# Optimization experiments

Measured on AMD Instinct MI355X. Metric: run time of the kernel, lower is better.

## Reference

```python
import jax, jax.numpy as jnp
import numpy as np

N = 50000        # nodes
E_RAND = 800000  # random edges (self-loops appended -> E = 850000)
H = 8            # num_heads
D = 32           # h_feat_dim
IN = 128         # in_feat_dim
SM = 256         # sm_dim
SP = 128         # sp_dim
NEG_SLOPE = 0.2  # DGL GATv2Conv default


def setup_inputs() -> dict:
    key = jax.random.key(0)
    ks = jax.random.split(key, 16)
    s = 0.05
    self_loops = jnp.arange(N, dtype=jnp.int32)
    return {
        "sm_feats": jax.random.normal(ks[0], (N, SM), jnp.float32),
        "sp_feats": jax.random.normal(ks[1], (N, SP), jnp.float32),
        "src": jnp.concatenate([jax.random.randint(ks[2], (E_RAND,), 0, N, jnp.int32), self_loops]),
        "dst": jnp.concatenate([jax.random.randint(ks[3], (E_RAND,), 0, N, jnp.int32), self_loops]),
        # T1 / T2 linears
        "T1_w": jax.random.normal(ks[4], (SM, IN), jnp.float32) * s,
        "T1_b": jnp.zeros((IN,), jnp.float32),
        "T2_w": jax.random.normal(ks[5], (SP, IN), jnp.float32) * s,
        "T2_b": jnp.zeros((IN,), jnp.float32),
        # GATv2 layer 1: in = 2*IN
        "g1_src_w": jax.random.normal(ks[6], (2 * IN, H * D), jnp.float32) * s,
        "g1_dst_w": jax.random.normal(ks[7], (2 * IN, H * D), jnp.float32) * s,
        "g1_attn": jax.random.normal(ks[8], (H, D), jnp.float32) * s,
        "g1_bias": jnp.zeros((H * D,), jnp.float32),
        # GATv2 layer 2: in = D (after head-mean)
        "g2_src_w": jax.random.normal(ks[9], (D, H * D), jnp.float32) * s,
        "g2_dst_w": jax.random.normal(ks[10], (D, H * D), jnp.float32) * s,
        "g2_attn": jax.random.normal(ks[11], (H, D), jnp.float32) * s,
        "g2_bias": jnp.zeros((H * D,), jnp.float32),
    }


def gatv2_conv(x, src, dst, w_src, w_dst, attn, bias):
    # DGL GATv2Conv (share_weights=False, bias=True, no residual/activation)
    feat_src = (x @ w_src).reshape(-1, H, D)   # [N,H,D]
    feat_dst = (x @ w_dst).reshape(-1, H, D)   # [N,H,D]
    e = jax.nn.leaky_relu(feat_src[src] + feat_dst[dst], NEG_SLOPE)  # [E,H,D]
    score = jnp.einsum('ehd,hd->eh', e, attn)  # [E,H]
    # edge softmax over incoming edges per destination (self-loops ensure non-empty)
    smax = jax.ops.segment_max(score, dst, num_segments=N)           # [N,H]
    ex = jnp.exp(score - smax[dst])
    denom = jax.ops.segment_sum(ex, dst, num_segments=N)             # [N,H]
    alpha = ex / denom[dst]                                          # [E,H]
    out = jax.ops.segment_sum(alpha[:, :, None] * feat_src[src], dst, num_segments=N)  # [N,H,D]
    return out + bias.reshape(1, H, D)


def reference(sm_feats, sp_feats, src, dst,
              T1_w, T1_b, T2_w, T2_b,
              g1_src_w, g1_dst_w, g1_attn, g1_bias,
              g2_src_w, g2_dst_w, g2_attn, g2_bias):
    in_feat = jnp.concatenate([sm_feats @ T1_w + T1_b,
                               sp_feats @ T2_w + T2_b], axis=1)      # [N, 2*IN]
    h = gatv2_conv(in_feat, src, dst, g1_src_w, g1_dst_w, g1_attn, g1_bias)
    h = jax.nn.elu(h).mean(axis=1)                                   # [N, D]
    h = gatv2_conv(h, src, dst, g2_src_w, g2_dst_w, g2_attn, g2_bias)
    return h.mean(axis=1)                                            # [N, D]
```

## Files before the change

kernel.cpp:

```cpp
#include <hip/hip_runtime.h>
#include <hip/hip_fp16.h>


typedef unsigned int uint32;
typedef unsigned short u16;
typedef float f32x4 __attribute__((ext_vector_type(4)));
typedef _Float16 f16x2 __attribute__((ext_vector_type(2)));
typedef _Float16 f16x8 __attribute__((ext_vector_type(8)));

union H2 { f16x2 v; uint32 u; };

__device__ __forceinline__ int wave_incl_scan(int x) {
  int lane = threadIdx.x & 63;
#pragma unroll
  for (int off = 1; off < 64; off <<= 1) {
    int t = __shfl_up(x, off, 64);
    if (lane >= off) x += t;
  }
  return x;
}

__global__ __launch_bounds__(256) void k_deg(const int* __restrict__ dst, int* __restrict__ deg, int E) {
  int e = blockIdx.x * 256 + threadIdx.x;
  if (e < E) atomicAdd(&deg[dst[e]], 1);
}

__global__ __launch_bounds__(256) void k_blkscan(const int* __restrict__ in, int* __restrict__ out,
                                                 int* __restrict__ blksum, int n) {
  __shared__ int wsum[4];
  int tid = threadIdx.x;
  int i0 = blockIdx.x * 1024 + tid * 4;
  int v0 = 0, v1 = 0, v2 = 0, v3 = 0;
  if (i0 + 3 < n) {
    int4 t = *(const int4*)(in + i0);
    v0 = t.x; v1 = t.y; v2 = t.z; v3 = t.w;
  } else {
    if (i0 < n) v0 = in[i0];
    if (i0 + 1 < n) v1 = in[i0 + 1];
    if (i0 + 2 < n) v2 = in[i0 + 2];
    if (i0 + 3 < n) v3 = in[i0 + 3];
  }
  int ts = v0 + v1 + v2 + v3;
  int incl = wave_incl_scan(ts);
  int lane = tid & 63, wid = tid >> 6;
  if (lane == 63) wsum[wid] = incl;
  __syncthreads();
  if (tid == 0) {
    int a = wsum[0], b = wsum[1], c = wsum[2], d = wsum[3];
    wsum[0] = 0; wsum[1] = a; wsum[2] = a + b; wsum[3] = a + b + c;
    blksum[blockIdx.x] = a + b + c + d;
  }
  __syncthreads();
  int excl = wsum[wid] + incl - ts;
  if (i0 + 3 < n) {
    int4 o; o.x = excl; o.y = excl + v0; o.z = excl + v0 + v1; o.w = excl + v0 + v1 + v2;
    *(int4*)(out + i0) = o;
  } else {
    if (i0 < n) out[i0] = excl;
    if (i0 + 1 < n) out[i0 + 1] = excl + v0;
    if (i0 + 2 < n) out[i0 + 2] = excl + v0 + v1;
    if (i0 + 3 < n) out[i0 + 3] = excl + v0 + v1 + v2;
  }
}

__global__ void k_scan_top(int* __restrict__ bs, int G) {
  int lane = threadIdx.x;
  int base = 0;
  for (int s = 0; s < G; s += 64) {
    int i = s + lane;
    int v = (i < G) ? bs[i] : 0;
    int incl = wave_incl_scan(v);
    if (i < G) bs[i] = base + incl - v;
    base += __shfl(incl, 63, 64);
  }
}

__global__ __launch_bounds__(256) void k_addoff(int* __restrict__ rp, const int* __restrict__ bs, int n, int Etot) {
  int i = blockIdx.x * 256 + threadIdx.x;
  if (i < n) rp[i] += bs[i >> 10];
  if (i == 0) rp[n] = Etot;
}

__global__ __launch_bounds__(256) void k_fill(const int* __restrict__ src, const int* __restrict__ dst,
                                              const int* __restrict__ rp, int* __restrict__ cnt,
                                              int* __restrict__ csr_src, int E) {
  int e = blockIdx.x * 256 + threadIdx.x;
  if (e < E) {
    int d = dst[e];
    int p = rp[d] + atomicAdd(&cnt[d], 1);
    csr_src[p] = src[e];
  }
}

__global__ __launch_bounds__(256) void k_precomb(const float* __restrict__ T1w, const float* __restrict__ T1b,
                                                 const float* __restrict__ T2w, const float* __restrict__ T2b,
                                                 const float* __restrict__ G1, const float* __restrict__ G2,
                                                 __half* __restrict__ Bf, float* __restrict__ cvec) {
  int bb = blockIdx.x;
  const float* G = (bb < 385) ? G1 : G2;
  int off = (bb < 385) ? 0 : 256;
  int r = (bb < 385) ? bb : bb - 385;
  int j = threadIdx.x;
  float acc = 0.f;
  if (r < 256) {
    for (int m = 0; m < 128; m++) acc += T1w[r * 128 + m] * G[m * 256 + j];
  } else if (r < 384) {
    int rr = r - 256;
    for (int m = 0; m < 128; m++) acc += T2w[rr * 128 + m] * G[(128 + m) * 256 + j];
  } else {
    for (int m = 0; m < 128; m++) acc += T1b[m] * G[m * 256 + j] + T2b[m] * G[(128 + m) * 256 + j];
    cvec[off + j] = acc;
    return;
  }
  int k = r, colabs = off + j;
  int kt = k >> 5, lq = (k >> 3) & 3, j8 = k & 7;
  int cb = colabs >> 7, colr = colabs & 127, ni = colr >> 4, lr = colr & 15;
  size_t idx = ((size_t)(((cb * 12 + kt) * 8 + ni) * 4 + lq) * 16 + lr) * 8 + j8;
  Bf[idx] = __float2half(acc);
}

#define GLL(GP, LP)                                                     \
  __builtin_amdgcn_global_load_lds(                                     \
      (const __attribute__((address_space(1))) void*)(GP),              \
      (__attribute__((address_space(3))) void*)(LP), 16, 0, 0)

__global__ __launch_bounds__(256, 4) void k_gemm(const float* __restrict__ sm, const float* __restrict__ sp,
                                                 const u16* __restrict__ Bf, const float* __restrict__ cvec,
                                                 __half* __restrict__ fs, __half* __restrict__ fd, int N) {
  __shared__ u16 BFl[3 * 4096];
  int tid = threadIdx.x, w = tid >> 6, l = tid & 63;
  int lr = l & 15, lq = l >> 4;
  int L = blockIdx.x;
  int x = L & 7, m = L >> 3;
  int cb = m & 3;
  int rb = x + 8 * (m >> 2);
  int col0 = cb * 128, row0 = rb * 128;
  if (row0 >= N) return;
  int r0 = row0 + w * 32 + lr;
  int r1 = r0 + 16;
  int c0 = r0 < N ? r0 : N - 1;
  int c1 = r1 < N ? r1 : N - 1;
  const float* psm0 = sm + (size_t)c0 * 256 + lq * 8;
  const float* psm1 = sm + (size_t)c1 * 256 + lq * 8;
  const float* psp0 = sp + (size_t)c0 * 128 + lq * 8;
  const float* psp1 = sp + (size_t)c1 * 128 + lq * 8;

  f32x4 acc[2][8];
#pragma unroll
  for (int mt = 0; mt < 2; mt++)
#pragma unroll
    for (int ni = 0; ni < 8; ni++) acc[mt][ni] = (f32x4){0.f, 0.f, 0.f, 0.f};

#define STAGE_B(S, BUF)                                                 \
  {                                                                     \
    size_t g0 = (size_t)(cb * 12 + (S)) * 4096;                         \
    _Pragma("unroll") for (int i = 0; i < 2; i++) {                     \
      int c = i * 256 + tid;                                            \
      int lb = (BUF)*4096 + (i * 4 + w) * 512;                          \
      GLL(Bf + g0 + (size_t)c * 8, &BFl[lb]);                           \
    }                                                                   \
  }

#define LOADA(P, D)                                                     \
  {                                                                     \
    const float* _g0 = ((P) < 8) ? (psm0 + (P)*32) : (psp0 + ((P)-8) * 32); \
    const float* _g1 = ((P) < 8) ? (psm1 + (P)*32) : (psp1 + ((P)-8) * 32); \
    D[0] = *(const float4*)_g0;                                         \
    D[1] = *(const float4*)(_g0 + 4);                                   \
    D[2] = *(const float4*)_g1;                                         \
    D[3] = *(const float4*)(_g1 + 4);                                   \
  }

  float4 Aa[4], Ab[4];
  LOADA(0, Aa);
  STAGE_B(0, 0);
  STAGE_B(1, 1);
  asm volatile("s_waitcnt vmcnt(2)" ::: "memory");
  __builtin_amdgcn_sched_barrier(0);
  __builtin_amdgcn_s_barrier();

#pragma unroll
  for (int st = 0; st < 12; st++) {
    const int slot = st % 3;
    const float4* Dc = (st & 1) ? Ab : Aa;
    float4* Dn = (st & 1) ? Aa : Ab;
    if (st < 11) LOADA(st + 1, Dn);
    if (st < 10) STAGE_B(st + 2, (st + 2) % 3);
    f16x8 a0, a1;
    a0[0] = (_Float16)Dc[0].x; a0[1] = (_Float16)Dc[0].y;
    a0[2] = (_Float16)Dc[0].z; a0[3] = (_Float16)Dc[0].w;
    a0[4] = (_Float16)Dc[1].x; a0[5] = (_Float16)Dc[1].y;
    a0[6] = (_Float16)Dc[1].z; a0[7] = (_Float16)Dc[1].w;
    a1[0] = (_Float16)Dc[2].x; a1[1] = (_Float16)Dc[2].y;
    a1[2] = (_Float16)Dc[2].z; a1[3] = (_Float16)Dc[2].w;
    a1[4] = (_Float16)Dc[3].x; a1[5] = (_Float16)Dc[3].y;
    a1[6] = (_Float16)Dc[3].z; a1[7] = (_Float16)Dc[3].w;
#pragma unroll
    for (int ni = 0; ni < 8; ni++) {
      int lo = slot * 4096 + (ni * 64 + l) * 8;
      f16x8 bf = *(const f16x8*)&BFl[lo];
      acc[0][ni] = __builtin_amdgcn_mfma_f32_16x16x32_f16(a0, bf, acc[0][ni], 0, 0, 0);
      acc[1][ni] = __builtin_amdgcn_mfma_f32_16x16x32_f16(a1, bf, acc[1][ni], 0, 0, 0);
    }
    if (st < 10) {
      asm volatile("s_waitcnt vmcnt(6)" ::: "memory");
    } else if (st == 10) {
      asm volatile("s_waitcnt vmcnt(4)" ::: "memory");
    }
    if (st < 11) {
      __builtin_amdgcn_sched_barrier(0);
      __builtin_amdgcn_s_barrier();
    }
  }

#pragma unroll
  for (int mt = 0; mt < 2; mt++) {
    int rbr = row0 + w * 32 + mt * 16 + lq * 4;
#pragma unroll
    for (int ni = 0; ni < 8; ni++) {
      int c = col0 + ni * 16 + lr;
      float cv = cvec[c];
      __half* op = fs; int cc = c;
      if (c >= 256) { op = fd; cc = c - 256; }
#pragma unroll
      for (int r = 0; r < 4; r++) {
        int rr = rbr + r;
        if (rr < N) op[(size_t)rr * 256 + cc] = __float2half(acc[mt][ni][r] + cv);
      }
    }
  }
#undef STAGE_B
#undef LOADA
}

__global__ __launch_bounds__(256) void k_feat2(const float* __restrict__ h, const float* __restrict__ Ws,
                                               const float* __restrict__ Wd, __half* __restrict__ fs,
                                               __half* __restrict__ fd, int N) {
  int j = threadIdx.x;
  int n0 = blockIdx.x * 32;
  float ws[32], wd[32];
#pragma unroll
  for (int k = 0; k < 32; k++) {
    ws[k] = Ws[k * 256 + j];
    wd[k] = Wd[k * 256 + j];
  }
  int nend = n0 + 32; if (nend > N) nend = N;
#pragma unroll 2
  for (int n = n0; n < nend; n++) {
    const float* hr = h + (size_t)n * 32;
    float as = 0.f, ad = 0.f;
#pragma unroll
    for (int k = 0; k < 32; k++) {
      float hv = hr[k];
      as += hv * ws[k];
      ad += hv * wd[k];
    }
    fs[(size_t)n * 256 + j] = __float2half(as);
    fd[(size_t)n * 256 + j] = __float2half(ad);
  }
}

template <int FINAL>
__global__ __launch_bounds__(256) void k_edge(const uint4* __restrict__ fs4, const uint4* __restrict__ fd4,
                                              const int* __restrict__ csr_src, const int* __restrict__ rp,
                                              const float* __restrict__ attn, const float* __restrict__ bias,
                                              float* __restrict__ out, int N) {
  int n = blockIdx.x * 4 + (threadIdx.x >> 6);
  if (n >= N) return;
  int lane = threadIdx.x & 63;
  int lh = lane & 31;
  float4 a0 = ((const float4*)attn)[lh * 2];
  float4 a1 = ((const float4*)attn)[lh * 2 + 1];
  H2 AV01, AV23, AV45, AV67;
  AV01.v = (f16x2){(_Float16)a0.x, (_Float16)a0.y};
  AV23.v = (f16x2){(_Float16)a0.z, (_Float16)a0.w};
  AV45.v = (f16x2){(_Float16)a1.x, (_Float16)a1.y};
  AV67.v = (f16x2){(_Float16)a1.z, (_Float16)a1.w};
  const f16x2 c02 = {(_Float16)0.2f, (_Float16)0.2f};
  uint4 yu = fd4[(size_t)n * 32 + lh];
  H2 Y01, Y23, Y45, Y67;
  Y01.u = yu.x; Y23.u = yu.y; Y45.u = yu.z; Y67.u = yu.w;
  int beg = rp[n], end = rp[n + 1];
  float den = 0.f;
  float acc[8] = {0.f, 0.f, 0.f, 0.f, 0.f, 0.f, 0.f, 0.f};

  auto pair1 = [&](uint4 xu, bool tail) {
    H2 Xa, Xb, Xc, Xd;
    Xa.u = xu.x; Xb.u = xu.y; Xc.u = xu.z; Xd.u = xu.w;
    f16x2 e0 = Xa.v + Y01.v, e1 = Xb.v + Y23.v, e2 = Xc.v + Y45.v, e3 = Xd.v + Y67.v;
    f16x2 t0 = __builtin_elementwise_max(e0, e0 * c02);
    f16x2 t1 = __builtin_elementwise_max(e1, e1 * c02);
    f16x2 t2 = __builtin_elementwise_max(e2, e2 * c02);
    f16x2 t3 = __builtin_elementwise_max(e3, e3 * c02);
    float p = __builtin_amdgcn_fdot2(t0, AV01.v, 0.f, false);
    p = __builtin_amdgcn_fdot2(t1, AV23.v, p, false);
    p = __builtin_amdgcn_fdot2(t2, AV45.v, p, false);
    p = __builtin_amdgcn_fdot2(t3, AV67.v, p, false);
    p += __shfl_xor(p, 1, 64);
    p += __shfl_xor(p, 2, 64);
    float wgt = __expf(p);
    if (tail && lane >= 32) wgt = 0.f;
    den += wgt;
    acc[0] += wgt * (float)Xa.v.x; acc[1] += wgt * (float)Xa.v.y;
    acc[2] += wgt * (float)Xb.v.x; acc[3] += wgt * (float)Xb.v.y;
    acc[4] += wgt * (float)Xc.v.x; acc[5] += wgt * (float)Xc.v.y;
    acc[6] += wgt * (float)Xd.v.x; acc[7] += wgt * (float)Xd.v.y;
  };

  int e = beg;
  int np = (end - beg) >> 1;
  if (np > 0) {
    int sA = csr_src[e], sB = csr_src[e + 1];
    int s = (lane < 32) ? sA : sB;
    uint4 xcur = fs4[(size_t)s * 32 + lh];
    for (int q = 1; q < np; q++) {
      int eb = e + 2 * q;
      int tA = csr_src[eb], tB = csr_src[eb + 1];
      int t = (lane < 32) ? tA : tB;
      uint4 xnext = fs4[(size_t)t * 32 + lh];
      pair1(xcur, false);
      xcur = xnext;
    }
    pair1(xcur, false);
    e += 2 * np;
  }
  if (e < end) {
    int sA = csr_src[e];
    uint4 xu = fs4[(size_t)sA * 32 + lh];
    pair1(xu, true);
  }

  den += __shfl_xor(den, 32, 64);
#pragma unroll
  for (int j = 0; j < 8; j++) acc[j] += __shfl_xor(acc[j], 32, 64);
  float invd = 1.f / den;
  float4 b0 = ((const float4*)bias)[lh * 2];
  float4 b1 = ((const float4*)bias)[lh * 2 + 1];
  float bj[8] = {b0.x, b0.y, b0.z, b0.w, b1.x, b1.y, b1.z, b1.w};
#pragma unroll
  for (int j = 0; j < 8; j++) {
    float v = acc[j] * invd + bj[j];
    if (!FINAL) v = v > 0.f ? v : expm1f(v);
    acc[j] = v;
  }
#pragma unroll
  for (int mask = 4; mask <= 16; mask <<= 1)
#pragma unroll
    for (int j = 0; j < 8; j++) acc[j] += __shfl_xor(acc[j], mask, 64);
  if (lane < 4) {
    float4 o0 = {acc[0] * 0.125f, acc[1] * 0.125f, acc[2] * 0.125f, acc[3] * 0.125f};
    float4 o1 = {acc[4] * 0.125f, acc[5] * 0.125f, acc[6] * 0.125f, acc[7] * 0.125f};
    ((float4*)out)[(size_t)n * 8 + lane * 2] = o0;
    ((float4*)out)[(size_t)n * 8 + lane * 2 + 1] = o1;
  }
}

extern "C" void kernel_launch(void* const* d_in, const int* in_sizes, int n_in,
                              void* d_out, int out_size, void* d_ws, size_t ws_size,
                              hipStream_t stream) {
  const float* sm  = (const float*)d_in[0];
  const float* sp  = (const float*)d_in[1];
  const int*   src = (const int*)d_in[2];
  const int*   dst = (const int*)d_in[3];
  const float* T1w = (const float*)d_in[4];
  const float* T1b = (const float*)d_in[5];
  const float* T2w = (const float*)d_in[6];
  const float* T2b = (const float*)d_in[7];
  const float* g1sw = (const float*)d_in[8];
  const float* g1dw = (const float*)d_in[9];
  const float* g1a  = (const float*)d_in[10];
  const float* g1b  = (const float*)d_in[11];
  const float* g2sw = (const float*)d_in[12];
  const float* g2dw = (const float*)d_in[13];
  const float* g2a  = (const float*)d_in[14];
  const float* g2b  = (const float*)d_in[15];
  const int N = in_sizes[1] / 128;
  const int E = in_sizes[2];
  float* out = (float*)d_out;

  size_t off = 0;
  char* wsb = (char*)d_ws;
  auto alloc = [&](size_t bytes) -> void* {
    void* p = wsb + off;
    off += (bytes + 255) & ~(size_t)255;
    return p;
  };
  __half* Bf  = (__half*)alloc((size_t)512 * 384 * 2);
  float* cvec  = (float*)alloc(512 * 4);
  int* deg     = (int*)alloc((size_t)N * 4);
  int* cnt     = (int*)alloc((size_t)N * 4);
  int* row_ptr = (int*)alloc((size_t)(N + 1) * 4);
  int* blksum  = (int*)alloc(4096 * 4);
  int* csr_src = (int*)alloc((size_t)E * 4);
  __half* fs   = (__half*)alloc((size_t)N * 256 * 2);
  __half* fd   = (__half*)alloc((size_t)N * 256 * 2);
  float* hmid  = (float*)alloc((size_t)N * 32 * 4);
  (void)ws_size; (void)n_in; (void)out_size;

  (void)hipMemsetAsync(deg, 0, (size_t)N * 4, stream);
  (void)hipMemsetAsync(cnt, 0, (size_t)N * 4, stream);

  k_deg<<<(E + 255) / 256, 256, 0, stream>>>(dst, deg, E);
  int nblk = (N + 1023) / 1024;
  k_blkscan<<<nblk, 256, 0, stream>>>(deg, row_ptr, blksum, N);
  k_scan_top<<<1, 64, 0, stream>>>(blksum, nblk);
  k_addoff<<<(N + 255) / 256, 256, 0, stream>>>(row_ptr, blksum, N, E);
  k_fill<<<(E + 255) / 256, 256, 0, stream>>>(src, dst, row_ptr, cnt, csr_src, E);

  k_precomb<<<770, 256, 0, stream>>>(T1w, T1b, T2w, T2b, g1sw, g1dw, Bf, cvec);

  int rbs = (N + 127) / 128;
  int rbp = (rbs + 7) & ~7;
  k_gemm<<<dim3(rbp * 4), 256, 0, stream>>>(sm, sp, (const u16*)Bf, cvec, fs, fd, N);
  k_edge<0><<<(N + 3) / 4, 256, 0, stream>>>((const uint4*)fs, (const uint4*)fd, csr_src, row_ptr, g1a, g1b, hmid, N);

  k_feat2<<<(N + 31) / 32, 256, 0, stream>>>(hmid, g2sw, g2dw, fs, fd, N);
  k_edge<1><<<(N + 3) / 4, 256, 0, stream>>>((const uint4*)fs, (const uint4*)fd, csr_src, row_ptr, g2a, g2b, out, N);
}
```

Measured before the change: 456.5 us.

## Fuse prefix scan into one kernel and load GEMM B operand directly from global

Replaces the three-kernel degree scan (block scan, top scan, add offsets) with a single 1024-thread block that scans all nodes in chunks, removing two launches and the block-sum buffer. In the GEMM, drops LDS staging of the B operand via global_load_lds and the per-stage barriers, reading B fragments straight from global memory (a small matrix likely held in cache) for each MFMA. The single-block scan serializes about 13 chunks on one CU. Direct global B loads trade barrier and LDS traffic for extra memory latency on the critical MFMA path.

```diff
diff --git a/kernel.cpp b/kernel.cpp
--- a/kernel.cpp
+++ b/kernel.cpp
@@ -25,60 +25,55 @@
   if (e < E) atomicAdd(&deg[dst[e]], 1);
 }
 
-__global__ __launch_bounds__(256) void k_blkscan(const int* __restrict__ in, int* __restrict__ out,
-                                                 int* __restrict__ blksum, int n) {
-  __shared__ int wsum[4];
-  int tid = threadIdx.x;
-  int i0 = blockIdx.x * 1024 + tid * 4;
-  int v0 = 0, v1 = 0, v2 = 0, v3 = 0;
-  if (i0 + 3 < n) {
-    int4 t = *(const int4*)(in + i0);
-    v0 = t.x; v1 = t.y; v2 = t.z; v3 = t.w;
-  } else {
-    if (i0 < n) v0 = in[i0];
-    if (i0 + 1 < n) v1 = in[i0 + 1];
-    if (i0 + 2 < n) v2 = in[i0 + 2];
-    if (i0 + 3 < n) v3 = in[i0 + 3];
-  }
-  int ts = v0 + v1 + v2 + v3;
-  int incl = wave_incl_scan(ts);
-  int lane = tid & 63, wid = tid >> 6;
-  if (lane == 63) wsum[wid] = incl;
+__global__ __launch_bounds__(1024) void k_scan1(const int* __restrict__ deg, int* __restrict__ rp,
+                                                int n, int Etot) {
+  __shared__ int wpart[16];
+  __shared__ int sbase;
+  int tid = threadIdx.x, lane = tid & 63, wid = tid >> 6;
+  if (tid == 0) sbase = 0;
   __syncthreads();
-  if (tid == 0) {
-    int a = wsum[0], b = wsum[1], c = wsum[2], d = wsum[3];
-    wsum[0] = 0; wsum[1] = a; wsum[2] = a + b; wsum[3] = a + b + c;
-    blksum[blockIdx.x] = a + b + c + d;
-  }
-  __syncthreads();
-  int excl = wsum[wid] + incl - ts;
-  if (i0 + 3 < n) {
-    int4 o; o.x = excl; o.y = excl + v0; o.z = excl + v0 + v1; o.w = excl + v0 + v1 + v2;
-    *(int4*)(out + i0) = o;
-  } else {
-    if (i0 < n) out[i0] = excl;
-    if (i0 + 1 < n) out[i0 + 1] = excl + v0;
-    if (i0 + 2 < n) out[i0 + 2] = excl + v0 + v1;
-    if (i0 + 3 < n) out[i0 + 3] = excl + v0 + v1 + v2;
-  }
-}
-
-__global__ void k_scan_top(int* __restrict__ bs, int G) {
-  int lane = threadIdx.x;
-  int base = 0;
-  for (int s = 0; s < G; s += 64) {
-    int i = s + lane;
-    int v = (i < G) ? bs[i] : 0;
-    int incl = wave_incl_scan(v);
-    if (i < G) bs[i] = base + incl - v;
-    base += __shfl(incl, 63, 64);
-  }
-}
-
-__global__ __launch_bounds__(256) void k_addoff(int* __restrict__ rp, const int* __restrict__ bs, int n, int Etot) {
-  int i = blockIdx.x * 256 + threadIdx.x;
-  if (i < n) rp[i] += bs[i >> 10];
-  if (i == 0) rp[n] = Etot;
+  for (int c0 = 0; c0 < n; c0 += 4096) {
+    int i0 = c0 + tid * 4;
+    int v0 = 0, v1 = 0, v2 = 0, v3 = 0;
+    if (i0 + 3 < n) {
+      int4 t = *(const int4*)(deg + i0);
+      v0 = t.x; v1 = t.y; v2 = t.z; v3 = t.w;
+    } else {
+      if (i0 < n) v0 = deg[i0];
+      if (i0 + 1 < n) v1 = deg[i0 + 1];
+      if (i0 + 2 < n) v2 = deg[i0 + 2];
+      if (i0 + 3 < n) v3 = deg[i0 + 3];
+    }
+    int ts = v0 + v1 + v2 + v3;
+    int incl = wave_incl_scan(ts);
+    if (lane == 63) wpart[wid] = incl;
+    __syncthreads();
+    if (wid == 0 && lane < 16) {
+      int xv = wpart[lane];
+#pragma unroll
+      for (int off = 1; off < 16; off <<= 1) {
+        int t = __shfl_up(xv, off, 64);
+        if (lane >= off) xv += t;
+      }
+      wpart[lane] = xv;
+    }
+    __syncthreads();
+    int tot = wpart[15];
+    int base = sbase + (wid ? wpart[wid - 1] : 0);
+    int excl = base + incl - ts;
+    if (i0 + 3 < n) {
+      int4 o; o.x = excl; o.y = excl + v0; o.z = excl + v0 + v1; o.w = excl + v0 + v1 + v2;
+      *(int4*)(rp + i0) = o;
+    } else {
+      if (i0 < n) rp[i0] = excl;
+      if (i0 + 1 < n) rp[i0 + 1] = excl + v0;
+      if (i0 + 2 < n) rp[i0 + 2] = excl + v0 + v1;
+      if (i0 + 3 < n) rp[i0 + 3] = excl + v0 + v1 + v2;
+    }
+    __syncthreads();
+    if (tid == 0) sbase += tot;
+  }
+  if (tid == 0) rp[n] = Etot;
 }
 
 __global__ __launch_bounds__(256) void k_fill(const int* __restrict__ src, const int* __restrict__ dst,
@@ -119,15 +114,9 @@
   Bf[idx] = __float2half(acc);
 }
 
-#define GLL(GP, LP)                                                     \
-  __builtin_amdgcn_global_load_lds(                                     \
-      (const __attribute__((address_space(1))) void*)(GP),              \
-      (__attribute__((address_space(3))) void*)(LP), 16, 0, 0)
-
 __global__ __launch_bounds__(256, 4) void k_gemm(const float* __restrict__ sm, const float* __restrict__ sp,
                                                  const u16* __restrict__ Bf, const float* __restrict__ cvec,
                                                  __half* __restrict__ fs, __half* __restrict__ fd, int N) {
-  __shared__ u16 BFl[3 * 4096];
   int tid = threadIdx.x, w = tid >> 6, l = tid & 63;
   int lr = l & 15, lq = l >> 4;
   int L = blockIdx.x;
@@ -144,22 +133,13 @@
   const float* psm1 = sm + (size_t)c1 * 256 + lq * 8;
   const float* psp0 = sp + (size_t)c0 * 128 + lq * 8;
   const float* psp1 = sp + (size_t)c1 * 128 + lq * 8;
+  const u16* bp = Bf + (size_t)cb * 49152 + (size_t)l * 8;
 
   f32x4 acc[2][8];
 #pragma unroll
   for (int mt = 0; mt < 2; mt++)
 #pragma unroll
     for (int ni = 0; ni < 8; ni++) acc[mt][ni] = (f32x4){0.f, 0.f, 0.f, 0.f};
-
-#define STAGE_B(S, BUF)                                                 \
-  {                                                                     \
-    size_t g0 = (size_t)(cb * 12 + (S)) * 4096;                         \
-    _Pragma("unroll") for (int i = 0; i < 2; i++) {                     \
-      int c = i * 256 + tid;                                            \
-      int lb = (BUF)*4096 + (i * 4 + w) * 512;                          \
-      GLL(Bf + g0 + (size_t)c * 8, &BFl[lb]);                           \
-    }                                                                   \
-  }
 
 #define LOADA(P, D)                                                     \
   {                                                                     \
@@ -173,19 +153,12 @@
 
   float4 Aa[4], Ab[4];
   LOADA(0, Aa);
-  STAGE_B(0, 0);
-  STAGE_B(1, 1);
-  asm volatile("s_waitcnt vmcnt(2)" ::: "memory");
-  __builtin_amdgcn_sched_barrier(0);
-  __builtin_amdgcn_s_barrier();
 
 #pragma unroll
   for (int st = 0; st < 12; st++) {
-    const int slot = st % 3;
     const float4* Dc = (st & 1) ? Ab : Aa;
     float4* Dn = (st & 1) ? Aa : Ab;
     if (st < 11) LOADA(st + 1, Dn);
-    if (st < 10) STAGE_B(st + 2, (st + 2) % 3);
     f16x8 a0, a1;
     a0[0] = (_Float16)Dc[0].x; a0[1] = (_Float16)Dc[0].y;
     a0[2] = (_Float16)Dc[0].z; a0[3] = (_Float16)Dc[0].w;
@@ -197,19 +170,9 @@
     a1[6] = (_Float16)Dc[3].z; a1[7] = (_Float16)Dc[3].w;
 #pragma unroll
     for (int ni = 0; ni < 8; ni++) {
-      int lo = slot * 4096 + (ni * 64 + l) * 8;
-      f16x8 bf = *(const f16x8*)&BFl[lo];
+      f16x8 bf = *(const f16x8*)(bp + st * 4096 + ni * 512);
       acc[0][ni] = __builtin_amdgcn_mfma_f32_16x16x32_f16(a0, bf, acc[0][ni], 0, 0, 0);
       acc[1][ni] = __builtin_amdgcn_mfma_f32_16x16x32_f16(a1, bf, acc[1][ni], 0, 0, 0);
-    }
-    if (st < 10) {
-      asm volatile("s_waitcnt vmcnt(6)" ::: "memory");
-    } else if (st == 10) {
-      asm volatile("s_waitcnt vmcnt(4)" ::: "memory");
-    }
-    if (st < 11) {
-      __builtin_amdgcn_sched_barrier(0);
-      __builtin_amdgcn_s_barrier();
     }
   }
 
@@ -229,7 +192,6 @@
       }
     }
   }
-#undef STAGE_B
 #undef LOADA
 }
 
@@ -390,7 +352,6 @@
   int* deg     = (int*)alloc((size_t)N * 4);
   int* cnt     = (int*)alloc((size_t)N * 4);
   int* row_ptr = (int*)alloc((size_t)(N + 1) * 4);
-  int* blksum  = (int*)alloc(4096 * 4);
   int* csr_src = (int*)alloc((size_t)E * 4);
   __half* fs   = (__half*)alloc((size_t)N * 256 * 2);
   __half* fd   = (__half*)alloc((size_t)N * 256 * 2);
@@ -401,10 +362,7 @@
   (void)hipMemsetAsync(cnt, 0, (size_t)N * 4, stream);
 
   k_deg<<<(E + 255) / 256, 256, 0, stream>>>(dst, deg, E);
-  int nblk = (N + 1023) / 1024;
-  k_blkscan<<<nblk, 256, 0, stream>>>(deg, row_ptr, blksum, N);
-  k_scan_top<<<1, 64, 0, stream>>>(blksum, nblk);
-  k_addoff<<<(N + 255) / 256, 256, 0, stream>>>(row_ptr, blksum, N, E);
+  k_scan1<<<1, 1024, 0, stream>>>(deg, row_ptr, N, E);
   k_fill<<<(E + 255) / 256, 256, 0, stream>>>(src, dst, row_ptr, cnt, csr_src, E);
 
   k_precomb<<<770, 256, 0, stream>>>(T1w, T1b, T2w, T2b, g1sw, g1dw, Bf, cvec);
```

New measurement: 481.8 us. 5.6% more time.
